# Performance work log

Measured on AMD Instinct MI355X. Metric: run time of the kernel, lower is better.

## Reference

```python
import jax, jax.numpy as jnp
import numpy as np
import math

B, R, C = 4, 512, 512
E, H, D, M, F = 256, 16, 16, 16, 512  # embed, heads, qkv_dim, ms_hidden, ff_hidden
EPS = 1e-5


def setup_inputs() -> dict:
    key = jax.random.key(0)
    ks = jax.random.split(key, 20)
    s = lambda fan_in: 1.0 / math.sqrt(fan_in)
    u = lambda k, shape, lim: jax.random.uniform(k, shape, jnp.float32, -lim, lim)
    mix1_init = (1 / 2) ** 0.5
    mix2_init = (1 / 16) ** 0.5
    return {
        "row_emb": jax.random.normal(ks[0], (B, R, E), jnp.float32),
        "col_emb": jax.random.normal(ks[1], (B, C, E), jnp.float32),
        "cost_mat": jax.random.uniform(ks[2], (B, R, C), jnp.float32),
        "Wq": u(ks[3], (E, H * D), s(E)),
        "Wk": u(ks[4], (E, H * D), s(E)),
        "Wv": u(ks[5], (E, H * D), s(E)),
        "mix1_w": u(ks[6], (H, 2, M), mix1_init),
        "mix1_b": u(ks[7], (H, M), mix1_init),
        "mix2_w": u(ks[8], (H, M, 1), mix2_init),
        "mix2_b": u(ks[9], (H, 1), mix2_init),
        "Wc": u(ks[10], (H * D, E), s(H * D)),
        "bc": u(ks[11], (E,), s(H * D)),
        "W1": u(ks[12], (E, F), s(E)),
        "b1": u(ks[13], (F,), s(E)),
        "W2": u(ks[14], (F, E), s(F)),
        "b2": u(ks[15], (E,), s(F)),
        "g1": jnp.ones((E,), jnp.float32),
        "be1": jnp.zeros((E,), jnp.float32),
        "g2": jnp.ones((E,), jnp.float32),
        "be2": jnp.zeros((E,), jnp.float32),
    }


def _instance_norm(x, gamma, beta):
    # InstanceNorm1d on x permuted to (B, E, L): normalize over seq dim per (b, channel)
    mean = jnp.mean(x, axis=1, keepdims=True)          # [B,1,E]
    var = jnp.mean((x - mean) ** 2, axis=1, keepdims=True)
    return (x - mean) * jax.lax.rsqrt(var + EPS) * gamma + beta


def reference(row_emb, col_emb, cost_mat, Wq, Wk, Wv, mix1_w, mix1_b, mix2_w,
              mix2_b, Wc, bc, W1, b1, W2, b2, g1, be1, g2, be2):
    # QKV projections, split heads: [B,L,H*D] -> [B,H,L,D]
    q = (row_emb @ Wq).reshape(B, R, H, D).transpose(0, 2, 1, 3)
    k = (col_emb @ Wk).reshape(B, C, H, D).transpose(0, 2, 1, 3)
    v = (col_emb @ Wv).reshape(B, C, H, D).transpose(0, 2, 1, 3)

    dot = jnp.einsum('bhrd,bhcd->bhrc', q, k) / math.sqrt(D)
    cost = jnp.broadcast_to(cost_mat[:, None, :, :], (B, H, R, C))
    two = jnp.stack((dot, cost), axis=-1)               # [B,H,R,C,2]

    # per-head 2 -> M -> 1 mixing MLP over scores
    ms1 = jnp.einsum('bhrcs,hsm->bhrcm', two, mix1_w) + mix1_b[None, :, None, None, :]
    ms1 = jax.nn.relu(ms1)
    mixed = jnp.einsum('bhrcm,hm->bhrc', ms1, mix2_w[:, :, 0]) + mix2_b[:, 0][None, :, None, None]

    weights = jax.nn.softmax(mixed, axis=-1)            # [B,H,R,C]
    out = jnp.einsum('bhrc,bhcd->bhrd', weights, v)
    out_concat = out.transpose(0, 2, 1, 3).reshape(B, R, H * D)

    mh = out_concat @ Wc + bc                           # multi_head_combine

    # TransformerFFN with instance norm
    x = _instance_norm(row_emb + mh, g1, be1)
    ffn = jax.nn.relu(x @ W1 + b1) @ W2 + b2
    return _instance_norm(x + ffn, g2, be2)
```

## Files before the change

kernel.cpp:

```cpp
#include <hip/hip_runtime.h>
#include <hip/hip_bf16.h>

typedef __hip_bfloat16 bf16;
typedef __hip_bfloat162 bf162;
typedef _Float16 f16;
typedef __attribute__((ext_vector_type(2))) _Float16 h2;
typedef __attribute__((ext_vector_type(4))) _Float16 f16x4;
typedef __attribute__((ext_vector_type(8))) short short8;
typedef __attribute__((ext_vector_type(4))) short short4v;
typedef __attribute__((ext_vector_type(4))) float f32x4;

#define B_ 4
#define R_ 512
#define C_ 512
#define E_ 256
#define H_ 16
#define D_ 16

__device__ __forceinline__ float b2f(bf16 x) { return __bfloat162float(x); }
__device__ __forceinline__ void stout(bf16* p, float v) { *p = __float2bfloat16(v); }
__device__ __forceinline__ void stout(f16* p, float v) { *p = (f16)v; }

__global__ __launch_bounds__(256) void transpose_cvt_kernel(
    const float* __restrict__ Wq, const float* __restrict__ Wk, const float* __restrict__ Wv,
    const float* __restrict__ Wc, const float* __restrict__ W1, const float* __restrict__ W2,
    bf16* __restrict__ WqT, bf16* __restrict__ WkT, bf16* __restrict__ WvT,
    bf16* __restrict__ WcT, bf16* __restrict__ W1T, bf16* __restrict__ W2T,
    float* __restrict__ statsZ)
{
    __shared__ bf16 tile[32][33];
    const int wsel = blockIdx.y;
    const int tx = blockIdx.x;
    if (wsel == 0 && tx >= 64) {
        const int idx = (tx - 64) * 256 + threadIdx.x;
        if (idx < 4096) statsZ[idx] = 0.f;
        return;
    }
    const float* src; bf16* dst; int K, N; float scl = 1.0f;
    switch (wsel) {
        case 0: src = Wq; dst = WqT; K = 256; N = 256; scl = 0.25f; break;
        case 1: src = Wk; dst = WkT; K = 256; N = 256; break;
        case 2: src = Wv; dst = WvT; K = 256; N = 256; break;
        case 3: src = Wc; dst = WcT; K = 256; N = 256; break;
        case 4: src = W1; dst = W1T; K = 256; N = 512; break;
        default: src = W2; dst = W2T; K = 512; N = 256; break;
    }
    const int ntiles = (K >> 5) * (N >> 5);
    if (tx >= ntiles) return;
    const int ncnt = N >> 5;
    const int tk = tx / ncnt, tn = tx % ncnt;
    const int c = threadIdx.x & 31, r = threadIdx.x >> 5;
#pragma unroll
    for (int i = 0; i < 4; i++)
        tile[r + i * 8][c] = __float2bfloat16(scl * src[(size_t)(tk * 32 + r + i * 8) * N + tn * 32 + c]);
    __syncthreads();
#pragma unroll
    for (int i = 0; i < 4; i++)
        dst[(size_t)(tn * 32 + r + i * 8) * K + tk * 32 + c] = tile[c][r + i * 8];
}

template <int AMODE, typename OT, int BM, int BN, bool BIAS, int RES, bool RELU, bool STATS>
__device__ __forceinline__ void mfma_gemm_body(
    const void* __restrict__ Ap, const bf16* __restrict__ BT,
    const float* __restrict__ bias, const void* __restrict__ Res,
    const float* __restrict__ normS, const float* __restrict__ normG, const float* __restrict__ normB,
    float* __restrict__ statsOut, OT* __restrict__ Cout,
    int M, int N, int K, int bx, int by)
{
    constexpr int MT = BM / 32, NT = BN / 32;
    constexpr int AEL = BM * 64 / 256, BEL = BN * 64 / 256;
    __shared__ __align__(16) bf16 As[BM * 80];
    __shared__ __align__(16) bf16 Bs[BN * 80];
    const int tid = threadIdx.x;
    const int wid = tid >> 6, lane = tid & 63;
    const int wm = wid >> 1, wn = wid & 1;
    const int fr = lane & 15, quad = lane >> 4;
    const int m0 = by * BM, n0 = bx * BN;
    const int arow = (AEL == 16) ? (tid >> 2) : (tid >> 3);
    const int akg  = (AEL == 16) ? ((tid & 3) << 4) : ((tid & 7) << 3);
    const int brow = (BEL == 16) ? (tid >> 2) : (tid >> 3);
    const int bkg  = (BEL == 16) ? ((tid & 3) << 4) : ((tid & 7) << 3);

    f32x4 acc[MT][NT];
#pragma unroll
    for (int mt = 0; mt < MT; mt++)
#pragma unroll
        for (int nt = 0; nt < NT; nt++) acc[mt][nt] = (f32x4){0.f, 0.f, 0.f, 0.f};

    for (int k0 = 0; k0 < K; k0 += 64) {
        if constexpr (AMODE == 0) {
            const short8* gp = (const short8*)((const bf16*)Ap + (size_t)(m0 + arow) * K + k0 + akg);
#pragma unroll
            for (int t8 = 0; t8 < AEL / 8; t8++) *(short8*)(&As[arow * 80 + akg + 8 * t8]) = gp[t8];
        } else if constexpr (AMODE == 1) {
            const float4* gp = (const float4*)((const float*)Ap + (size_t)(m0 + arow) * K + k0 + akg);
#pragma unroll
            for (int j = 0; j < AEL / 4; j++) {
                const float4 f = gp[j];
                *(bf162*)(&As[arow * 80 + akg + j * 4])     = __float22bfloat162_rn(make_float2(f.x, f.y));
                *(bf162*)(&As[arow * 80 + akg + j * 4 + 2]) = __float22bfloat162_rn(make_float2(f.z, f.w));
            }
        } else {
            const int bb = (m0 + arow) >> 9;
            const bf16* ap = (const bf16*)Ap + (size_t)(m0 + arow) * K + k0 + akg;
            bf16 tmp[AEL];
#pragma unroll
            for (int t8 = 0; t8 < AEL / 8; t8++) *(short8*)(tmp + 8 * t8) = ((const short8*)ap)[t8];
#pragma unroll
            for (int j = 0; j < AEL; j++) {
                const int e = k0 + akg + j;
                const float s = normS[bb * 256 + e], sq = normS[1024 + bb * 256 + e];
                const float mn = s * (1.f / 512.f);
                float var = sq * (1.f / 512.f) - mn * mn; var = fmaxf(var, 0.f);
                As[arow * 80 + akg + j] = __float2bfloat16(
                    (b2f(tmp[j]) - mn) * rsqrtf(var + 1e-5f) * normG[e] + normB[e]);
            }
        }
        {
            const short8* gp = (const short8*)(BT + (size_t)(n0 + brow) * K + k0 + bkg);
#pragma unroll
            for (int t8 = 0; t8 < BEL / 8; t8++) *(short8*)(&Bs[brow * 80 + bkg + 8 * t8]) = gp[t8];
        }
        __syncthreads();

        short8 af[MT][2], bfr[NT][2];
#pragma unroll
        for (int mt = 0; mt < MT; mt++) {
            const int ar = wm * (BM / 2) + mt * 16 + fr;
#pragma unroll
            for (int kh = 0; kh < 2; kh++)
                af[mt][kh] = *(const short8*)(&As[ar * 80 + quad * 8 + kh * 32]);
        }
#pragma unroll
        for (int nt = 0; nt < NT; nt++) {
            const int br = wn * (BN / 2) + nt * 16 + fr;
#pragma unroll
            for (int kh = 0; kh < 2; kh++)
                bfr[nt][kh] = *(const short8*)(&Bs[br * 80 + quad * 8 + kh * 32]);
        }
#pragma unroll
        for (int kh = 0; kh < 2; kh++)
#pragma unroll
            for (int mt = 0; mt < MT; mt++)
#pragma unroll
                for (int nt = 0; nt < NT; nt++)
                    acc[mt][nt] = __builtin_amdgcn_mfma_f32_16x16x32_bf16(
                        af[mt][kh], bfr[nt][kh], acc[mt][nt], 0, 0, 0);
        __syncthreads();
    }

    float vsum[NT], vss[NT];
#pragma unroll
    for (int nt = 0; nt < NT; nt++) { vsum[nt] = 0.f; vss[nt] = 0.f; }
#pragma unroll
    for (int mt = 0; mt < MT; mt++) {
#pragma unroll
        for (int nt = 0; nt < NT; nt++) {
#pragma unroll
            for (int i = 0; i < 4; i++) {
                const int row = m0 + wm * (BM / 2) + mt * 16 + quad * 4 + i;
                const int col = n0 + wn * (BN / 2) + nt * 16 + fr;
                float v = acc[mt][nt][i];
                if (BIAS) v += bias[col];
                if constexpr (RES == 1) v += ((const float*)Res)[(size_t)row * N + col];
                if constexpr (RES == 3) {
                    const int bb = row >> 9;
                    const float yv = b2f(((const bf16*)Res)[(size_t)row * N + col]);
                    const float s = normS[bb * 256 + col], sq = normS[1024 + bb * 256 + col];
                    const float mn = s * (1.f / 512.f);
                    float var = sq * (1.f / 512.f) - mn * mn; var = fmaxf(var, 0.f);
                    v += (yv - mn) * rsqrtf(var + 1e-5f) * normG[col] + normB[col];
                }
                if (RELU) v = fmaxf(v, 0.f);
                stout(&Cout[(size_t)row * N + col], v);
                if (STATS) { vsum[nt] += v; vss[nt] += v * v; }
            }
        }
    }
    if constexpr (STATS) {
        float* sred = (float*)As;
#pragma unroll
        for (int nt = 0; nt < NT; nt++) {
            float a = vsum[nt]; a += __shfl_xor(a, 16, 64); a += __shfl_xor(a, 32, 64);
            float c = vss[nt];  c += __shfl_xor(c, 16, 64); c += __shfl_xor(c, 32, 64);
            if (quad == 0) {
                const int cl = wn * (BN / 2) + nt * 16 + fr;
                sred[wm * (2 * BN) + cl * 2 + 0] = a;
                sred[wm * (2 * BN) + cl * 2 + 1] = c;
            }
        }
        __syncthreads();
        if (tid < 2 * BN) {
            const int cl = tid >> 1, w = tid & 1;
            const float tot = sred[cl * 2 + w] + sred[2 * BN + cl * 2 + w];
            atomicAdd(&statsOut[w * 1024 + (m0 >> 9) * 256 + n0 + cl], tot);
        }
    }
}

template <int AMODE, typename OT, int BM, int BN, bool BIAS, int RES, bool RELU, bool STATS>
__global__ __launch_bounds__(256) void mfma_gemm_kernel(
    const void* __restrict__ Ap, const bf16* __restrict__ BT,
    const float* __restrict__ bias, const void* __restrict__ Res,
    const float* __restrict__ normS, const float* __restrict__ normG, const float* __restrict__ normB,
    float* __restrict__ statsOut, OT* __restrict__ Cout, int M, int N, int K)
{
    mfma_gemm_body<AMODE, OT, BM, BN, BIAS, RES, RELU, STATS>(
        Ap, BT, bias, Res, normS, normG, normB, statsOut, Cout,
        M, N, K, blockIdx.x, blockIdx.y);
}

__global__ __launch_bounds__(256) void qkv_kernel(
    const float* __restrict__ rowE, const float* __restrict__ colE,
    const bf16* __restrict__ WqT, const bf16* __restrict__ WkT, const bf16* __restrict__ WvT,
    f16* __restrict__ qo, f16* __restrict__ ko, f16* __restrict__ vo)
{
    const int z = blockIdx.z;
    const float* A = (z == 0) ? rowE : colE;
    const bf16* BT = (z == 0) ? WqT : (z == 1) ? WkT : WvT;
    f16* out = (z == 0) ? qo : (z == 1) ? ko : vo;
    mfma_gemm_body<1, f16, 32, 64, false, 0, false, false>(
        A, BT, nullptr, nullptr, nullptr, nullptr, nullptr, nullptr, out,
        2048, 256, 256, blockIdx.x, blockIdx.y);
}

__global__ __launch_bounds__(256) void attn_kernel(
    const f16* __restrict__ q, const f16* __restrict__ k, const f16* __restrict__ v,
    const float* __restrict__ cost, const float* __restrict__ m1w, const float* __restrict__ m1b,
    const float* __restrict__ m2w, const float* __restrict__ m2b,
    bf16* __restrict__ sa)
{
    __shared__ __align__(16) short kbuf[512 * 16];
    __shared__ __align__(16) _Float16 vbufT[16 * 520];

    const int rt = blockIdx.x, h = blockIdx.y, b = blockIdx.z;
    const int tid = threadIdx.x, wid = tid >> 6, lane = tid & 63;
    const int quad = lane >> 4, fr = lane & 15;
    const int row_m = rt * 64 + wid * 16 + fr;

    const f16x4 qf = *(const f16x4*)(q + (size_t)(b * R_ + row_m) * 256 + h * 16 + (quad << 2));

    {
        const int lc0 = tid >> 1, dp = (tid & 1) * 8;
        const size_t gbase = (size_t)(b * C_) * 256 + h * 16 + dp;
#pragma unroll
        for (int it = 0; it < 4; it++) {
            const int lc = it * 128 + lc0;
            const size_t g = gbase + (size_t)lc * 256;
            *(short8*)(&kbuf[lc * 16 + (dp ^ ((lc & 1) << 3))]) = *(const short8*)(k + g);
            const short8 vv = *(const short8*)(v + g);
#pragma unroll
            for (int u = 0; u < 8; u++) vbufT[(dp + u) * 520 + lc] = ((const _Float16*)&vv)[u];
        }
    }

    h2 w1a2[8], w1b2[8], b1h[8], w2p[8];
#pragma unroll
    for (int i = 0; i < 8; i++) {
        h2 t;
        t.x = (f16)m1w[h * 32 + 2 * i];      t.y = (f16)m1w[h * 32 + 2 * i + 1];      w1a2[i] = t;
        t.x = (f16)m1w[h * 32 + 16 + 2 * i]; t.y = (f16)m1w[h * 32 + 17 + 2 * i];     w1b2[i] = t;
        t.x = (f16)m1b[h * 16 + 2 * i];      t.y = (f16)m1b[h * 16 + 2 * i + 1];      b1h[i] = t;
        t.x = (f16)m2w[h * 16 + 2 * i];      t.y = (f16)m2w[h * 16 + 2 * i + 1];      w2p[i] = t;
    }
    const float b2v = m2b[h];
    const h2 zero2 = (h2)(f16)0;

    const float* crow = cost + (size_t)(b * R_ + row_m) * C_;
    float4 cf[2][8];
#pragma unroll
    for (int t = 0; t < 8; t++) cf[0][t] = *(const float4*)(crow + t * 16 + (quad << 2));

    __syncthreads();

    f32x4 oaccT = (f32x4){0.f, 0.f, 0.f, 0.f};
    float lsum = 0.f, m_run = -3.0e30f;

#pragma unroll
    for (int cs = 0; cs < 4; cs++) {
        if (cs < 3) {
#pragma unroll
            for (int t = 0; t < 8; t++)
                cf[(cs + 1) & 1][t] = *(const float4*)(crow + (cs + 1) * 128 + t * 16 + (quad << 2));
        }
        f32x4 sc[8];
#pragma unroll
        for (int t = 0; t < 8; t++) {
            const int c = cs * 128 + t * 16 + fr;
            const f16x4 kf = *(const f16x4*)(&kbuf[c * 16 + ((quad << 2) ^ ((fr & 1) << 3))]);
            sc[t] = __builtin_amdgcn_mfma_f32_16x16x16f16(kf, qf, (f32x4){0.f, 0.f, 0.f, 0.f}, 0, 0, 0);
        }
#pragma unroll
        for (int t = 0; t < 8; t++) {
            const float4 cq = cf[cs & 1][t];
            const float carr[4] = {cq.x, cq.y, cq.z, cq.w};
#pragma unroll
            for (int i = 0; i < 4; i++) {
                const f16 doth = (f16)sc[t][i], csth = (f16)carr[i];
                h2 dot2; dot2.x = doth; dot2.y = doth;
                h2 cst2; cst2.x = csth; cst2.y = csth;
                h2 acc2 = zero2;
#pragma unroll
                for (int mm = 0; mm < 8; mm++) {
                    h2 tt = dot2 * w1a2[mm] + b1h[mm];
                    tt = cst2 * w1b2[mm] + tt;
                    tt = __builtin_elementwise_max(tt, zero2);
                    acc2 = tt * w2p[mm] + acc2;
                }
                sc[t][i] = b2v + (float)acc2.x + (float)acc2.y;
            }
        }
        float mx = fmaxf(fmaxf(sc[0][0], sc[0][1]), fmaxf(sc[0][2], sc[0][3]));
#pragma unroll
        for (int t = 1; t < 8; t++)
            mx = fmaxf(mx, fmaxf(fmaxf(sc[t][0], sc[t][1]), fmaxf(sc[t][2], sc[t][3])));
        mx = fmaxf(mx, __shfl_xor(mx, 16, 64));
        mx = fmaxf(mx, __shfl_xor(mx, 32, 64));
        const float mnew = fmaxf(m_run, mx);
        const float fac = __expf(m_run - mnew);
        m_run = mnew;
        lsum *= fac;
        oaccT[0] *= fac; oaccT[1] *= fac; oaccT[2] *= fac; oaccT[3] *= fac;

#pragma unroll
        for (int p = 0; p < 8; p++) {
            f16x4 pf;
#pragma unroll
            for (int j = 0; j < 4; j++) {
                const float e = __expf(sc[p][j] - m_run);
                lsum += e;
                pf[j] = (f16)e;
            }
            const f16x4 vf = *(const f16x4*)(&vbufT[fr * 520 + cs * 128 + p * 16 + (quad << 2)]);
            oaccT = __builtin_amdgcn_mfma_f32_16x16x16f16(vf, pf, oaccT, 0, 0, 0);
        }
    }

    lsum += __shfl_xor(lsum, 16, 64);
    lsum += __shfl_xor(lsum, 32, 64);
    const float inv = 1.f / lsum;
    short4v o;
#pragma unroll
    for (int i = 0; i < 4; i++) o[i] = __builtin_bit_cast(short, __float2bfloat16(oaccT[i] * inv));
    *(short4v*)((short*)sa + (size_t)(b * R_ + row_m) * 256 + h * 16 + (quad << 2)) = o;
}

__global__ __launch_bounds__(256) void apply_in2_kernel(
    const bf16* __restrict__ xin, const float* __restrict__ stats,
    const float* __restrict__ g, const float* __restrict__ be, float* __restrict__ outp)
{
    const int base = (blockIdx.x * 256 + threadIdx.x) * 4;
    const int b = base >> 17;
    const bf162* xp = (const bf162*)(xin + base);
    const float2 x0 = __bfloat1622float2(xp[0]), x1 = __bfloat1622float2(xp[1]);
    const float xv[4] = {x0.x, x0.y, x1.x, x1.y};
    float4 rr;
    float* rp = (float*)&rr;
#pragma unroll
    for (int j = 0; j < 4; j++) {
        const int e = (base & 255) + j;
        const float s = stats[b * 256 + e], sq = stats[1024 + b * 256 + e];
        const float mn = s * (1.f / 512.f);
        float var = sq * (1.f / 512.f) - mn * mn; var = fmaxf(var, 0.f);
        rp[j] = (xv[j] - mn) * rsqrtf(var + 1e-5f) * g[e] + be[e];
    }
    *(float4*)(outp + base) = rr;
}

extern "C" void kernel_launch(void* const* d_in, const int* in_sizes, int n_in,
                              void* d_out, int out_size, void* d_ws, size_t ws_size,
                              hipStream_t stream)
{
    (void)in_sizes; (void)n_in; (void)out_size; (void)ws_size;
    const float* row_emb = (const float*)d_in[0];
    const float* col_emb = (const float*)d_in[1];
    const float* cost    = (const float*)d_in[2];
    const float* Wq  = (const float*)d_in[3];
    const float* Wk  = (const float*)d_in[4];
    const float* Wv  = (const float*)d_in[5];
    const float* m1w = (const float*)d_in[6];
    const float* m1b = (const float*)d_in[7];
    const float* m2w = (const float*)d_in[8];
    const float* m2b = (const float*)d_in[9];
    const float* Wc  = (const float*)d_in[10];
    const float* bc  = (const float*)d_in[11];
    const float* W1  = (const float*)d_in[12];
    const float* b1  = (const float*)d_in[13];
    const float* W2  = (const float*)d_in[14];
    const float* b2  = (const float*)d_in[15];
    const float* g1  = (const float*)d_in[16];
    const float* be1 = (const float*)d_in[17];
    const float* g2  = (const float*)d_in[18];
    const float* be2 = (const float*)d_in[19];
    float* out = (float*)d_out;

    char* w = (char*)d_ws;
    const size_t MB = 1u << 20;
    f16*  sq  = (f16*)(w + 0 * MB);
    f16*  sk  = (f16*)(w + 1 * MB);
    f16*  sv  = (f16*)(w + 2 * MB);
    bf16* sa  = (bf16*)(w + 3 * MB);
    bf16* sy  = (bf16*)(w + 4 * MB);
    bf16* st  = (bf16*)(w + 5 * MB);
    bf16* shm = (bf16*)(w + 6 * MB);
    bf16* WqT = (bf16*)(w + 8 * MB);
    bf16* WkT = WqT + 65536;
    bf16* WvT = WkT + 65536;
    bf16* WcT = WvT + 65536;
    bf16* W1T = WcT + 65536;
    bf16* W2T = W1T + 131072;
    float* stats1 = (float*)(w + 9 * MB);
    float* stats2 = stats1 + 2048;

    const dim3 blk(256);

    transpose_cvt_kernel<<<dim3(128, 6), blk, 0, stream>>>(
        Wq, Wk, Wv, Wc, W1, W2, WqT, WkT, WvT, WcT, W1T, W2T, stats1);

    qkv_kernel<<<dim3(4, 64, 3), blk, 0, stream>>>(row_emb, col_emb, WqT, WkT, WvT, sq, sk, sv);

    attn_kernel<<<dim3(8, 16, 4), blk, 0, stream>>>(
        sq, sk, sv, cost, m1w, m1b, m2w, m2b, sa);

    mfma_gemm_kernel<0, bf16, 32, 32, true, 1, false, true><<<dim3(8, 64), blk, 0, stream>>>(
        sa, WcT, bc, row_emb, nullptr, nullptr, nullptr, stats1, sy, 2048, 256, 256);

    mfma_gemm_kernel<2, bf16, 32, 64, true, 0, true, false><<<dim3(8, 64), blk, 0, stream>>>(
        sy, W1T, b1, nullptr, stats1, g1, be1, nullptr, shm, 2048, 512, 256);

    mfma_gemm_kernel<0, bf16, 32, 32, true, 3, false, true><<<dim3(8, 64), blk, 0, stream>>>(
        shm, W2T, b2, sy, stats1, g1, be1, stats2, st, 2048, 256, 512);

    apply_in2_kernel<<<dim3(512), blk, 0, stream>>>(st, stats2, g2, be2, out);
}
```

Measured before the change: 153.2 us.

## Fuse combine, FFN GEMMs and final norm into one cooperative kernel

Replaces the three post-attention GEMM launches and the final instance-norm kernel with a single cooperative kernel. Grid-wide syncs separate the phases, and each phase reuses the same 512-block tiling. The goal is to remove launch overhead and inter-kernel gaps. In exchange it adds grid barrier cost, and it depends on all 512 blocks being co-resident, with launch_bounds set to 2 blocks per CU.

```diff
diff --git a/kernel.cpp b/kernel.cpp
--- a/kernel.cpp
+++ b/kernel.cpp
@@ -1,5 +1,8 @@
 #include <hip/hip_runtime.h>
 #include <hip/hip_bf16.h>
+#include <hip/hip_cooperative_groups.h>
+
+namespace cg = cooperative_groups;
 
 typedef __hip_bfloat16 bf16;
 typedef __hip_bfloat162 bf162;
@@ -198,18 +201,6 @@
     }
 }
 
-template <int AMODE, typename OT, int BM, int BN, bool BIAS, int RES, bool RELU, bool STATS>
-__global__ __launch_bounds__(256) void mfma_gemm_kernel(
-    const void* __restrict__ Ap, const bf16* __restrict__ BT,
-    const float* __restrict__ bias, const void* __restrict__ Res,
-    const float* __restrict__ normS, const float* __restrict__ normG, const float* __restrict__ normB,
-    float* __restrict__ statsOut, OT* __restrict__ Cout, int M, int N, int K)
-{
-    mfma_gemm_body<AMODE, OT, BM, BN, BIAS, RES, RELU, STATS>(
-        Ap, BT, bias, Res, normS, normG, normB, statsOut, Cout,
-        M, N, K, blockIdx.x, blockIdx.y);
-}
-
 __global__ __launch_bounds__(256) void qkv_kernel(
     const float* __restrict__ rowE, const float* __restrict__ colE,
     const bf16* __restrict__ WqT, const bf16* __restrict__ WkT, const bf16* __restrict__ WvT,
@@ -345,26 +336,48 @@
     *(short4v*)((short*)sa + (size_t)(b * R_ + row_m) * 256 + h * 16 + (quad << 2)) = o;
 }
 
-__global__ __launch_bounds__(256) void apply_in2_kernel(
-    const bf16* __restrict__ xin, const float* __restrict__ stats,
-    const float* __restrict__ g, const float* __restrict__ be, float* __restrict__ outp)
-{
-    const int base = (blockIdx.x * 256 + threadIdx.x) * 4;
-    const int b = base >> 17;
-    const bf162* xp = (const bf162*)(xin + base);
-    const float2 x0 = __bfloat1622float2(xp[0]), x1 = __bfloat1622float2(xp[1]);
-    const float xv[4] = {x0.x, x0.y, x1.x, x1.y};
-    float4 rr;
-    float* rp = (float*)&rr;
-#pragma unroll
-    for (int j = 0; j < 4; j++) {
-        const int e = (base & 255) + j;
-        const float s = stats[b * 256 + e], sq = stats[1024 + b * 256 + e];
-        const float mn = s * (1.f / 512.f);
-        float var = sq * (1.f / 512.f) - mn * mn; var = fmaxf(var, 0.f);
-        rp[j] = (xv[j] - mn) * rsqrtf(var + 1e-5f) * g[e] + be[e];
-    }
-    *(float4*)(outp + base) = rr;
+__global__ __launch_bounds__(256, 2) void ffn_fused_kernel(
+    const bf16* __restrict__ sa, const bf16* __restrict__ WcT, const float* __restrict__ bc,
+    const float* __restrict__ row_emb,
+    const bf16* __restrict__ W1T, const float* __restrict__ b1,
+    const bf16* __restrict__ W2T, const float* __restrict__ b2,
+    const float* __restrict__ g1, const float* __restrict__ be1,
+    const float* __restrict__ g2, const float* __restrict__ be2,
+    float* __restrict__ stats1, float* __restrict__ stats2,
+    bf16* __restrict__ sy, bf16* __restrict__ shm, bf16* __restrict__ st,
+    float* __restrict__ outp)
+{
+    const int wg = blockIdx.x;
+    mfma_gemm_body<0, bf16, 32, 32, true, 1, false, true>(
+        sa, WcT, bc, row_emb, nullptr, nullptr, nullptr, stats1, sy,
+        2048, 256, 256, wg & 7, wg >> 3);
+    cg::this_grid().sync();
+    mfma_gemm_body<2, bf16, 32, 64, true, 0, true, false>(
+        sy, W1T, b1, nullptr, stats1, g1, be1, nullptr, shm,
+        2048, 512, 256, wg & 7, wg >> 3);
+    cg::this_grid().sync();
+    mfma_gemm_body<0, bf16, 32, 32, true, 3, false, true>(
+        shm, W2T, b2, sy, stats1, g1, be1, stats2, st,
+        2048, 256, 512, wg & 7, wg >> 3);
+    cg::this_grid().sync();
+    {
+        const int base = (wg * 256 + threadIdx.x) * 4;
+        const int b = base >> 17;
+        const bf162* xp = (const bf162*)(st + base);
+        const float2 x0 = __bfloat1622float2(xp[0]), x1 = __bfloat1622float2(xp[1]);
+        const float xv[4] = {x0.x, x0.y, x1.x, x1.y};
+        float4 rr;
+        float* rp = (float*)&rr;
+#pragma unroll
+        for (int j = 0; j < 4; j++) {
+            const int e = (base & 255) + j;
+            const float s = stats2[b * 256 + e], sq = stats2[1024 + b * 256 + e];
+            const float mn = s * (1.f / 512.f);
+            float var = sq * (1.f / 512.f) - mn * mn; var = fmaxf(var, 0.f);
+            rp[j] = (xv[j] - mn) * rsqrtf(var + 1e-5f) * g2[e] + be2[e];
+        }
+        *(float4*)(outp + base) = rr;
+    }
 }
 
 extern "C" void kernel_launch(void* const* d_in, const int* in_sizes, int n_in,
@@ -422,14 +435,14 @@
     attn_kernel<<<dim3(8, 16, 4), blk, 0, stream>>>(
         sq, sk, sv, cost, m1w, m1b, m2w, m2b, sa);
 
-    mfma_gemm_kernel<0, bf16, 32, 32, true, 1, false, true><<<dim3(8, 64), blk, 0, stream>>>(
-        sa, WcT, bc, row_emb, nullptr, nullptr, nullptr, stats1, sy, 2048, 256, 256);
-
-    mfma_gemm_kernel<2, bf16, 32, 64, true, 0, true, false><<<dim3(8, 64), blk, 0, stream>>>(
-        sy, W1T, b1, nullptr, stats1, g1, be1, nullptr, shm, 2048, 512, 256);
-
-    mfma_gemm_kernel<0, bf16, 32, 32, true, 3, false, true><<<dim3(8, 64), blk, 0, stream>>>(
-        shm, W2T, b2, sy, stats1, g1, be1, stats2, st, 2048, 256, 512);
-
-    apply_in2_kernel<<<dim3(512), blk, 0, stream>>>(st, stats2, g2, be2, out);
-}
+    {
+        void* args[] = {
+            (void*)&sa, (void*)&WcT, (void*)&bc, (void*)&row_emb,
+            (void*)&W1T, (void*)&b1, (void*)&W2T, (void*)&b2,
+            (void*)&g1, (void*)&be1, (void*)&g2, (void*)&be2,
+            (void*)&stats1, (void*)&stats2, (void*)&sy, (void*)&shm, (void*)&st, (void*)&out
+        };
+        hipLaunchCooperativeKernel((const void*)ffn_fused_kernel, dim3(512), dim3(256),
+                                   args, 0, stream);
+    }
+}
```

Result: slower. 335.6 us (+119.1%).

## Fuse FFN W1 and W2 GEMMs into one kernel keeping hidden tile in LDS

Applied to the files above, without the earlier changes.

Replaces the two separate FFN GEMM launches with a single kernel in which each block takes 16 rows. It applies instance norm 1 to the input, computes relu(xW1+b1) into shared memory, then multiplies by W2 and adds the residual and second-norm statistics. This removes the global round trip of the hidden activation and one launch. In exchange the grid shrinks to 128 blocks of 16 rows, and each block streams the full W1 and W2 from global memory with little weight reuse, which lowers parallelism on a large GPU.

```diff
diff --git a/kernel.cpp b/kernel.cpp
--- a/kernel.cpp
+++ b/kernel.cpp
@@ -343,6 +343,146 @@
 #pragma unroll
     for (int i = 0; i < 4; i++) o[i] = __builtin_bit_cast(short, __float2bfloat16(oaccT[i] * inv));
     *(short4v*)((short*)sa + (size_t)(b * R_ + row_m) * 256 + h * 16 + (quad << 2)) = o;
+}
+
+__global__ __launch_bounds__(256) void ffn12_kernel(
+    const bf16* __restrict__ sy, const bf16* __restrict__ W1T, const float* __restrict__ b1,
+    const bf16* __restrict__ W2T, const float* __restrict__ b2,
+    const float* __restrict__ stats1, const float* __restrict__ g1, const float* __restrict__ be1,
+    float* __restrict__ stats2, bf16* __restrict__ st)
+{
+    __shared__ __align__(16) bf16 As[16 * 264];
+    __shared__ __align__(16) bf16 hm[16 * 520];
+    __shared__ __align__(16) bf16 Bs[256 * 80];
+
+    const int tid = threadIdx.x, wid = tid >> 6, lane = tid & 63;
+    const int quad = lane >> 4, fr = lane & 15;
+    const int wn = wid;
+    const int m0 = blockIdx.x * 16;
+    const int bb = m0 >> 9;
+
+    {
+        const int arow = tid >> 4, ae0 = (tid & 15) << 4;
+        const bf16* ap = sy + (size_t)(m0 + arow) * 256 + ae0;
+        bf16 tmp[16];
+        *(short8*)(tmp)     = ((const short8*)ap)[0];
+        *(short8*)(tmp + 8) = ((const short8*)ap)[1];
+#pragma unroll
+        for (int j = 0; j < 16; j++) {
+            const int e = ae0 + j;
+            const float s = stats1[bb * 256 + e], sq2 = stats1[1024 + bb * 256 + e];
+            const float mn = s * (1.f / 512.f);
+            float var = sq2 * (1.f / 512.f) - mn * mn; var = fmaxf(var, 0.f);
+            As[arow * 264 + e] = __float2bfloat16(
+                (b2f(tmp[j]) - mn) * rsqrtf(var + 1e-5f) * g1[e] + be1[e]);
+        }
+    }
+    __syncthreads();
+
+#pragma unroll
+    for (int nb = 0; nb < 4; nb++) {
+        f32x4 acc[2];
+        acc[0] = (f32x4){0.f, 0.f, 0.f, 0.f};
+        acc[1] = (f32x4){0.f, 0.f, 0.f, 0.f};
+        for (int k0 = 0; k0 < 256; k0 += 64) {
+#pragma unroll
+            for (int rr = 0; rr < 4; rr++) {
+                const int row = rr * 32 + (tid >> 3), kg = (tid & 7) << 3;
+                *(short8*)(&Bs[row * 80 + kg]) =
+                    *(const short8*)(W1T + (size_t)(nb * 128 + row) * 256 + k0 + kg);
+            }
+            __syncthreads();
+            short8 af[2], bfr[2][2];
+#pragma unroll
+            for (int kh = 0; kh < 2; kh++)
+                af[kh] = *(const short8*)(&As[fr * 264 + k0 + quad * 8 + kh * 32]);
+#pragma unroll
+            for (int nt = 0; nt < 2; nt++) {
+                const int br = wn * 32 + nt * 16 + fr;
+#pragma unroll
+                for (int kh = 0; kh < 2; kh++)
+                    bfr[nt][kh] = *(const short8*)(&Bs[br * 80 + quad * 8 + kh * 32]);
+            }
+#pragma unroll
+            for (int kh = 0; kh < 2; kh++)
+#pragma unroll
+                for (int nt = 0; nt < 2; nt++)
+                    acc[nt] = __builtin_amdgcn_mfma_f32_16x16x32_bf16(
+                        af[kh], bfr[nt][kh], acc[nt], 0, 0, 0);
+            __syncthreads();
+        }
+#pragma unroll
+        for (int nt = 0; nt < 2; nt++) {
+            const int coll = nb * 128 + wn * 32 + nt * 16 + fr;
+            const float bv = b1[coll];
+#pragma unroll
+            for (int i = 0; i < 4; i++)
+                hm[(quad * 4 + i) * 520 + coll] = __float2bfloat16(fmaxf(acc[nt][i] + bv, 0.f));
+        }
+    }
+    __syncthreads();
+
+    f32x4 acc[4];
+#pragma unroll
+    for (int nt = 0; nt < 4; nt++) acc[nt] = (f32x4){0.f, 0.f, 0.f, 0.f};
+    for (int k0 = 0; k0 < 512; k0 += 64) {
+#pragma unroll
+        for (int rr = 0; rr < 8; rr++) {
+            const int row = rr * 32 + (tid >> 3), kg = (tid & 7) << 3;
+            *(short8*)(&Bs[row * 80 + kg]) =
+                *(const short8*)(W2T + (size_t)row * 512 + k0 + kg);
+        }
+        __syncthreads();
+        short8 af[2], bfr[4][2];
+#pragma unroll
+        for (int kh = 0; kh < 2; kh++)
+            af[kh] = *(const short8*)(&hm[fr * 520 + k0 + quad * 8 + kh * 32]);
+#pragma unroll
+        for (int nt = 0; nt < 4; nt++) {
+            const int br = wn * 64 + nt * 16 + fr;
+#pragma unroll
+            for (int kh = 0; kh < 2; kh++)
+                bfr[nt][kh] = *(const short8*)(&Bs[br * 80 + quad * 8 + kh * 32]);
+        }
+#pragma unroll
+        for (int kh = 0; kh < 2; kh++)
+#pragma unroll
+            for (int nt = 0; nt < 4; nt++)
+                acc[nt] = __builtin_amdgcn_mfma_f32_16x16x32_bf16(
+                    af[kh], bfr[nt][kh], acc[nt], 0, 0, 0);
+        __syncthreads();
+    }
+
+    float vsum[4], vss[4];
+#pragma unroll
+    for (int nt = 0; nt < 4; nt++) { vsum[nt] = 0.f; vss[nt] = 0.f; }
+#pragma unroll
+    for (int nt = 0; nt < 4; nt++) {
+        const int col = wn * 64 + nt * 16 + fr;
+        const float s = stats1[bb * 256 + col], sq2 = stats1[1024 + bb * 256 + col];
+        const float mn = s * (1.f / 512.f);
+        float var = sq2 * (1.f / 512.f) - mn * mn; var = fmaxf(var, 0.f);
+        const float rs = rsqrtf(var + 1e-5f) * g1[col];
+        const float bev = be1[col], bv = b2[col];
+#pragma unroll
+        for (int i = 0; i < 4; i++) {
+            const int row = m0 + quad * 4 + i;
+            const float yv = b2f(sy[(size_t)row * 256 + col]);
+            float v = acc[nt][i] + bv + (yv - mn) * rs + bev;
+            st[(size_t)row * 256 + col] = __float2bfloat16(v);
+            vsum[nt] += v; vss[nt] += v * v;
+        }
+    }
+#pragma unroll
+    for (int nt = 0; nt < 4; nt++) {
+        float a = vsum[nt]; a += __shfl_xor(a, 16, 64); a += __shfl_xor(a, 32, 64);
+        float c = vss[nt];  c += __shfl_xor(c, 16, 64); c += __shfl_xor(c, 32, 64);
+        if (quad == 0) {
+            const int col = wn * 64 + nt * 16 + fr;
+            atomicAdd(&stats2[bb * 256 + col], a);
+            atomicAdd(&stats2[1024 + bb * 256 + col], c);
+        }
+    }
 }
 
 __global__ __launch_bounds__(256) void apply_in2_kernel(
@@ -402,7 +542,6 @@
     bf16* sa  = (bf16*)(w + 3 * MB);
     bf16* sy  = (bf16*)(w + 4 * MB);
     bf16* st  = (bf16*)(w + 5 * MB);
-    bf16* shm = (bf16*)(w + 6 * MB);
     bf16* WqT = (bf16*)(w + 8 * MB);
     bf16* WkT = WqT + 65536;
     bf16* WvT = WkT + 65536;
@@ -425,11 +564,8 @@
     mfma_gemm_kernel<0, bf16, 32, 32, true, 1, false, true><<<dim3(8, 64), blk, 0, stream>>>(
         sa, WcT, bc, row_emb, nullptr, nullptr, nullptr, stats1, sy, 2048, 256, 256);
 
-    mfma_gemm_kernel<2, bf16, 32, 64, true, 0, true, false><<<dim3(8, 64), blk, 0, stream>>>(
-        sy, W1T, b1, nullptr, stats1, g1, be1, nullptr, shm, 2048, 512, 256);
-
-    mfma_gemm_kernel<0, bf16, 32, 32, true, 3, false, true><<<dim3(8, 64), blk, 0, stream>>>(
-        shm, W2T, b2, sy, stats1, g1, be1, stats2, st, 2048, 256, 512);
+    ffn12_kernel<<<dim3(128), blk, 0, stream>>>(
+        sy, W1T, b1, W2T, b2, stats1, g1, be1, stats2, st);
 
     apply_in2_kernel<<<dim3(512), blk, 0, stream>>>(st, stats2, g2, be2, out);
 }
```

After: 159.7 us. 4.3% more time.

## Fuse weight transpose/convert into QKV projection kernel, dropping one launch

Applied to the files above, without the earlier changes.

Merges the weight transpose/convert kernel and the QKV GEMM into one launch. QKV blocks now read fp32 Wq/Wk/Wv directly and convert and transpose them into LDS on the fly, scaling Wq by 0.25. Spare blocks in the same grid transpose Wc/W1/W2 and zero the stats buffer. This removes one kernel launch and the serial dependency between weight prep and the QKV GEMM. In exchange, each QKV block redoes the fp32 weight reads and conversion, and its scattered 2-byte LDS transposed stores may cause bank conflicts.

```diff
diff --git a/kernel.cpp b/kernel.cpp
--- a/kernel.cpp
+++ b/kernel.cpp
@@ -20,44 +20,6 @@
 __device__ __forceinline__ float b2f(bf16 x) { return __bfloat162float(x); }
 __device__ __forceinline__ void stout(bf16* p, float v) { *p = __float2bfloat16(v); }
 __device__ __forceinline__ void stout(f16* p, float v) { *p = (f16)v; }
-
-__global__ __launch_bounds__(256) void transpose_cvt_kernel(
-    const float* __restrict__ Wq, const float* __restrict__ Wk, const float* __restrict__ Wv,
-    const float* __restrict__ Wc, const float* __restrict__ W1, const float* __restrict__ W2,
-    bf16* __restrict__ WqT, bf16* __restrict__ WkT, bf16* __restrict__ WvT,
-    bf16* __restrict__ WcT, bf16* __restrict__ W1T, bf16* __restrict__ W2T,
-    float* __restrict__ statsZ)
-{
-    __shared__ bf16 tile[32][33];
-    const int wsel = blockIdx.y;
-    const int tx = blockIdx.x;
-    if (wsel == 0 && tx >= 64) {
-        const int idx = (tx - 64) * 256 + threadIdx.x;
-        if (idx < 4096) statsZ[idx] = 0.f;
-        return;
-    }
-    const float* src; bf16* dst; int K, N; float scl = 1.0f;
-    switch (wsel) {
-        case 0: src = Wq; dst = WqT; K = 256; N = 256; scl = 0.25f; break;
-        case 1: src = Wk; dst = WkT; K = 256; N = 256; break;
-        case 2: src = Wv; dst = WvT; K = 256; N = 256; break;
-        case 3: src = Wc; dst = WcT; K = 256; N = 256; break;
-        case 4: src = W1; dst = W1T; K = 256; N = 512; break;
-        default: src = W2; dst = W2T; K = 512; N = 256; break;
-    }
-    const int ntiles = (K >> 5) * (N >> 5);
-    if (tx >= ntiles) return;
-    const int ncnt = N >> 5;
-    const int tk = tx / ncnt, tn = tx % ncnt;
-    const int c = threadIdx.x & 31, r = threadIdx.x >> 5;
-#pragma unroll
-    for (int i = 0; i < 4; i++)
-        tile[r + i * 8][c] = __float2bfloat16(scl * src[(size_t)(tk * 32 + r + i * 8) * N + tn * 32 + c]);
-    __syncthreads();
-#pragma unroll
-    for (int i = 0; i < 4; i++)
-        dst[(size_t)(tn * 32 + r + i * 8) * K + tk * 32 + c] = tile[c][r + i * 8];
-}
 
 template <int AMODE, typename OT, int BM, int BN, bool BIAS, int RES, bool RELU, bool STATS>
 __device__ __forceinline__ void mfma_gemm_body(
@@ -210,18 +172,113 @@
         M, N, K, blockIdx.x, blockIdx.y);
 }
 
-__global__ __launch_bounds__(256) void qkv_kernel(
+__global__ __launch_bounds__(256) void prep_qkv_kernel(
     const float* __restrict__ rowE, const float* __restrict__ colE,
-    const bf16* __restrict__ WqT, const bf16* __restrict__ WkT, const bf16* __restrict__ WvT,
+    const float* __restrict__ Wq, const float* __restrict__ Wk, const float* __restrict__ Wv,
+    const float* __restrict__ Wc, const float* __restrict__ W1, const float* __restrict__ W2,
+    bf16* __restrict__ WcT, bf16* __restrict__ W1T, bf16* __restrict__ W2T,
+    float* __restrict__ statsZ,
     f16* __restrict__ qo, f16* __restrict__ ko, f16* __restrict__ vo)
 {
-    const int z = blockIdx.z;
+    __shared__ __align__(16) short pool[32 * 80 + 64 * 80];
+    const int bid = blockIdx.x;
+    const int tid = threadIdx.x;
+
+    if (bid >= 768) {
+        const int spare = bid - 768;
+        if (spare >= 320) {
+            statsZ[(spare - 320) * 256 + tid] = 0.f;
+            return;
+        }
+        bf16 (*tile)[33] = (bf16(*)[33])pool;
+        const float* src; bf16* dst; int K, N, tix;
+        if (spare < 64)       { src = Wc; dst = WcT; K = 256; N = 256; tix = spare; }
+        else if (spare < 192) { src = W1; dst = W1T; K = 256; N = 512; tix = spare - 64; }
+        else                  { src = W2; dst = W2T; K = 512; N = 256; tix = spare - 192; }
+        const int ncnt = N >> 5;
+        const int tk = tix / ncnt, tn = tix % ncnt;
+        const int c = tid & 31, r = tid >> 5;
+#pragma unroll
+        for (int i = 0; i < 4; i++)
+            tile[r + i * 8][c] = __float2bfloat16(src[(size_t)(tk * 32 + r + i * 8) * N + tn * 32 + c]);
+        __syncthreads();
+#pragma unroll
+        for (int i = 0; i < 4; i++)
+            dst[(size_t)(tn * 32 + r + i * 8) * K + tk * 32 + c] = tile[c][r + i * 8];
+        return;
+    }
+
+    const int z = bid >> 8;
+    const int rem = bid & 255;
+    const int bx = rem & 3, by = rem >> 2;
     const float* A = (z == 0) ? rowE : colE;
-    const bf16* BT = (z == 0) ? WqT : (z == 1) ? WkT : WvT;
+    const float* W = (z == 0) ? Wq : (z == 1) ? Wk : Wv;
     f16* out = (z == 0) ? qo : (z == 1) ? ko : vo;
-    mfma_gemm_body<1, f16, 32, 64, false, 0, false, false>(
-        A, BT, nullptr, nullptr, nullptr, nullptr, nullptr, nullptr, out,
-        2048, 256, 256, blockIdx.x, blockIdx.y);
+    const float scl = (z == 0) ? 0.25f : 1.0f;
+
+    bf16* As = (bf16*)pool;
+    bf16* Bs = (bf16*)pool + 32 * 80;
+
+    const int wid = tid >> 6, lane = tid & 63;
+    const int wm = wid >> 1, wn = wid & 1;
+    const int fr = lane & 15, quad = lane >> 4;
+    const int m0 = by * 32, n0 = bx * 64;
+    const int arow = tid >> 3, akg = (tid & 7) << 3;
+    const int bkk = tid >> 2, bseg = (tid & 3) << 4;
+
+    f32x4 acc[2];
+    acc[0] = (f32x4){0.f, 0.f, 0.f, 0.f};
+    acc[1] = (f32x4){0.f, 0.f, 0.f, 0.f};
+
+    for (int k0 = 0; k0 < 256; k0 += 64) {
+        {
+            const float4* gp = (const float4*)(A + (size_t)(m0 + arow) * 256 + k0 + akg);
+#pragma unroll
+            for (int j = 0; j < 2; j++) {
+                const float4 f = gp[j];
+                *(bf162*)(&As[arow * 80 + akg + j * 4])     = __float22bfloat162_rn(make_float2(f.x, f.y));
+                *(bf162*)(&As[arow * 80 + akg + j * 4 + 2]) = __float22bfloat162_rn(make_float2(f.z, f.w));
+            }
+        }
+        {
+            const float* wp = W + (size_t)(k0 + bkk) * 256 + n0 + bseg;
+#pragma unroll
+            for (int j4 = 0; j4 < 4; j4++) {
+                const float4 f = *(const float4*)(wp + 4 * j4);
+                Bs[(bseg + 4 * j4 + 0) * 80 + bkk] = __float2bfloat16(scl * f.x);
+                Bs[(bseg + 4 * j4 + 1) * 80 + bkk] = __float2bfloat16(scl * f.y);
+                Bs[(bseg + 4 * j4 + 2) * 80 + bkk] = __float2bfloat16(scl * f.z);
+                Bs[(bseg + 4 * j4 + 3) * 80 + bkk] = __float2bfloat16(scl * f.w);
+            }
+        }
+        __syncthreads();
+        short8 af[2], bfr[2][2];
+#pragma unroll
+        for (int kh = 0; kh < 2; kh++)
+            af[kh] = *(const short8*)(&As[(wm * 16 + fr) * 80 + quad * 8 + kh * 32]);
+#pragma unroll
+        for (int nt = 0; nt < 2; nt++)
+#pragma unroll
+            for (int kh = 0; kh < 2; kh++)
+                bfr[nt][kh] = *(const short8*)(&Bs[(wn * 32 + nt * 16 + fr) * 80 + quad * 8 + kh * 32]);
+#pragma unroll
+        for (int kh = 0; kh < 2; kh++)
+#pragma unroll
+            for (int nt = 0; nt < 2; nt++)
+                acc[nt] = __builtin_amdgcn_mfma_f32_16x16x32_bf16(
+                    af[kh], bfr[nt][kh], acc[nt], 0, 0, 0);
+        __syncthreads();
+    }
+
+#pragma unroll
+    for (int nt = 0; nt < 2; nt++) {
+        const int col = n0 + wn * 32 + nt * 16 + fr;
+#pragma unroll
+        for (int i = 0; i < 4; i++) {
+            const int row = m0 + wm * 16 + quad * 4 + i;
+            out[(size_t)row * 256 + col] = (f16)acc[nt][i];
+        }
+    }
 }
 
 __global__ __launch_bounds__(256) void attn_kernel(
@@ -403,10 +460,7 @@
     bf16* sy  = (bf16*)(w + 4 * MB);
     bf16* st  = (bf16*)(w + 5 * MB);
     bf16* shm = (bf16*)(w + 6 * MB);
-    bf16* WqT = (bf16*)(w + 8 * MB);
-    bf16* WkT = WqT + 65536;
-    bf16* WvT = WkT + 65536;
-    bf16* WcT = WvT + 65536;
+    bf16* WcT = (bf16*)(w + 8 * MB);
     bf16* W1T = WcT + 65536;
     bf16* W2T = W1T + 131072;
     float* stats1 = (float*)(w + 9 * MB);
@@ -414,10 +468,9 @@
 
     const dim3 blk(256);
 
-    transpose_cvt_kernel<<<dim3(128, 6), blk, 0, stream>>>(
-        Wq, Wk, Wv, Wc, W1, W2, WqT, WkT, WvT, WcT, W1T, W2T, stats1);
-
-    qkv_kernel<<<dim3(4, 64, 3), blk, 0, stream>>>(row_emb, col_emb, WqT, WkT, WvT, sq, sk, sv);
+    prep_qkv_kernel<<<dim3(1104), blk, 0, stream>>>(
+        row_emb, col_emb, Wq, Wk, Wv, Wc, W1, W2,
+        WcT, W1T, W2T, stats1, sq, sk, sv);
 
     attn_kernel<<<dim3(8, 16, 4), blk, 0, stream>>>(
         sq, sk, sv, cost, m1w, m1b, m2w, m2b, sa);
```

After: 152.0 us. About the same (-0.7%).
